# Kernel optimization log

Hardware: AMD Instinct MI355X
Metric: run time of the kernel (lower is better)

Reference implementation:

```python
import jax, jax.numpy as jnp
import numpy as np

NUM_HEADS = 16

def _rope_tables(T, head_dim):
    # angular_freq: (1/1024)**linspace(0,1,head_dim//4), padded with head_dim//4 zeros
    af = (1.0 / 1024.0) ** jnp.linspace(0.0, 1.0, head_dim // 4, dtype=jnp.float32)
    af = jnp.concatenate([af, jnp.zeros(head_dim // 4, dtype=jnp.float32)])  # [head_dim//2]
    t = jnp.arange(T, dtype=jnp.float32)
    theta = t[:, None] * af[None, :]  # [T, head_dim//2]
    return jnp.cos(theta), jnp.sin(theta)

def _apply_rope(x_bthd, cos, sin):
    # x_bthd: [B,T,H,D]; cos/sin: [T,D//2]
    x1, x2 = jnp.split(x_bthd.astype(jnp.float32), 2, axis=-1)
    c = cos[None, :, None, :]
    s = sin[None, :, None, :]
    y1 = x1 * c + x2 * s
    y2 = -x1 * s + x2 * c
    return jnp.concatenate([y1, y2], axis=-1).astype(x_bthd.dtype)

def setup_inputs() -> dict:
    key = jax.random.key(0)
    k1, k2, k3 = jax.random.split(key, 3)
    B, T, C = 4, 2048, 1024
    std = 0.5 * C ** (-0.5)
    bound = (3.0 ** 0.5) * std
    x = jax.random.normal(k1, (B, T, C), dtype=jnp.float32)
    qkv_w = jax.random.uniform(k2, (3, C, C), dtype=jnp.float32, minval=-bound, maxval=bound)
    c_proj_w = 0.02 * jax.random.normal(k3, (C, C), dtype=jnp.float32)
    c_proj_b = jnp.zeros((C,), dtype=jnp.float32)
    return {"x": x, "qkv_w": qkv_w, "c_proj_w": c_proj_w, "c_proj_b": c_proj_b}

def reference(x, qkv_w, c_proj_w, c_proj_b):
    B, T, C = x.shape
    H = NUM_HEADS
    D = C // H
    # QKV projection: F.linear(x, qkv_w.flatten(end_dim=1)) -> x @ W.T
    qkv = jnp.einsum('btc,nc->btn', x, qkv_w.reshape(3 * C, C))  # [B,T,3C]
    qkv = qkv.reshape(B, T, 3 * H, D)
    q, k, v = jnp.split(qkv, 3, axis=-2)  # each [B,T,H,D]
    cos, sin = _rope_tables(T, D)
    q = _apply_rope(q, cos, sin)
    k = _apply_rope(k, cos, sin)
    # causal SDPA, scale 1/sqrt(D)
    scale = 1.0 / jnp.sqrt(jnp.float32(D))
    scores = jnp.einsum('bqhd,bkhd->bhqk', q, k) * scale  # [B,H,T,T]
    mask = jnp.tril(jnp.ones((T, T), dtype=bool))
    scores = jnp.where(mask[None, None], scores, jnp.finfo(scores.dtype).min)
    attn = jax.nn.softmax(scores, axis=-1)
    y = jnp.einsum('bhqk,bkhd->bqhd', attn, v).reshape(B, T, C)
    return y @ c_proj_w.T + c_proj_b
```

## Files before the change

kernel.cpp:

```cpp
#include <hip/hip_runtime.h>

typedef unsigned short ushort_t;
typedef __bf16 bf16x8 __attribute__((ext_vector_type(8)));
typedef unsigned short ushort8_t __attribute__((ext_vector_type(8)));
typedef unsigned short ushort4_t __attribute__((ext_vector_type(4)));
typedef float floatx4 __attribute__((ext_vector_type(4)));
typedef unsigned int uint4_t __attribute__((ext_vector_type(4)));
typedef unsigned int uint2_t __attribute__((ext_vector_type(2)));

__device__ __forceinline__ ushort_t f2bf(float f) {
    unsigned int u = __float_as_uint(f);
    u += 0x7FFFu + ((u >> 16) & 1u);
    return (ushort_t)(u >> 16);
}
__device__ __forceinline__ float bf2f(ushort_t b) {
    return __uint_as_float(((unsigned int)b) << 16);
}
__device__ __forceinline__ bf16x8 ld_frag(const ushort_t* p) {
    ushort8_t u = *(const ushort8_t*)p;
    return __builtin_bit_cast(bf16x8, u);
}
__device__ __forceinline__ unsigned pack_trunc(float lo, float hi) {
    return __builtin_amdgcn_perm(__float_as_uint(hi), __float_as_uint(lo), 0x07060302u);
}
__device__ __forceinline__ floatx4 mfma16(bf16x8 a, bf16x8 b, floatx4 c) {
    return __builtin_amdgcn_mfma_f32_16x16x32_bf16(a, b, c, 0, 0, 0);
}
__device__ __forceinline__ void async16(const ushort_t* g, ushort_t* l) {
    __builtin_amdgcn_global_load_lds((const __attribute__((address_space(1))) void*)g,
                                     (__attribute__((address_space(3))) void*)l, 16, 0, 0);
}

__global__ __launch_bounds__(256) void cvt_bf16(const float* __restrict__ src,
                                                ushort_t* __restrict__ dst, int n8) {
    int idx = blockIdx.x * 256 + threadIdx.x;
    if (idx >= n8) return;
    const float4* s = (const float4*)src + (size_t)idx * 2;
    float4 a = s[0], b = s[1];
    ushort8_t v;
    v[0] = f2bf(a.x); v[1] = f2bf(a.y); v[2] = f2bf(a.z); v[3] = f2bf(a.w);
    v[4] = f2bf(b.x); v[5] = f2bf(b.y); v[6] = f2bf(b.z); v[7] = f2bf(b.w);
    *(ushort8_t*)(dst + (size_t)idx * 8) = v;
}

template <typename TB, int MODE>
__global__ __launch_bounds__(256) void gemm_a(const ushort_t* __restrict__ A,
                                              const TB* __restrict__ B,
                                              const float* __restrict__ bias,
                                              void* __restrict__ Cout,
                                              ushort_t* __restrict__ vt,
                                              int M, int N, int K) {
    constexpr bool BF16B = (sizeof(TB) == 2);
    __shared__ __attribute__((aligned(16))) ushort_t As[128 * 32];
    __shared__ __attribute__((aligned(16))) ushort_t Bs[128 * 32];
    const int tid = threadIdx.x;
    const int lane = tid & 63, wave = tid >> 6;
    const int quad = lane >> 4, l16 = lane & 15;
    const int wm = wave & 1, wn = wave >> 1;
    const int m0 = blockIdx.y * 128, n0 = blockIdx.x * 128;

    const ushort_t* ga = A + (size_t)(m0 + wave * 32 + (lane >> 2)) * K + (lane & 3) * 8;
    ushort_t* la = As + wave * 1024;
    const ushort_t* gb16 = nullptr;
    if constexpr (BF16B)
        gb16 = (const ushort_t*)B + (size_t)(n0 + wave * 32 + (lane >> 2)) * K + (lane & 3) * 8;
    ushort_t* lb = Bs + wave * 1024;

    floatx4 acc[4][4] = {};

    for (int k0 = 0; k0 < K; k0 += 32) {
        __syncthreads();
        async16(ga + k0, la);
        async16(ga + k0 + (size_t)16 * K, la + 512);
        if constexpr (BF16B) {
            async16(gb16 + k0, lb);
            async16(gb16 + k0 + (size_t)16 * K, lb + 512);
        } else {
#pragma unroll
            for (int it = 0; it < 4; ++it) {
                int linear = it * 256 + tid;
                int row = linear >> 3, c = (linear & 7) * 4;
                const float* src = (const float*)B + (size_t)(n0 + row) * K + k0 + c;
                float4 f = *(const float4*)src;
                ushort4_t v;
                v.x = f2bf(f.x); v.y = f2bf(f.y); v.z = f2bf(f.z); v.w = f2bf(f.w);
                *(ushort4_t*)&Bs[row * 32 + c] = v;
            }
        }
        __syncthreads();

        bf16x8 af[4], bfr[4];
#pragma unroll
        for (int mt = 0; mt < 4; ++mt)
            af[mt] = ld_frag(&As[(wm * 64 + mt * 16 + l16) * 32 + quad * 8]);
#pragma unroll
        for (int nt = 0; nt < 4; ++nt)
            bfr[nt] = ld_frag(&Bs[(wn * 64 + nt * 16 + l16) * 32 + quad * 8]);
#pragma unroll
        for (int mt = 0; mt < 4; ++mt)
#pragma unroll
            for (int nt = 0; nt < 4; ++nt)
                acc[mt][nt] = mfma16(af[mt], bfr[nt], acc[mt][nt]);
    }

    if constexpr (MODE == 2) {
        if (n0 + wn * 64 < 2048) {
            float afreq = exp2f((float)l16 * (-10.0f / 15.0f));
#pragma unroll
            for (int mt = 0; mt < 4; ++mt) {
                int rowb = m0 + wm * 64 + mt * 16 + quad * 4;
#pragma unroll
                for (int r = 0; r < 4; ++r) {
                    int t = (rowb + r) & 2047;
                    float th = (float)t * afreq;
                    float sn = sinf(th), cs = cosf(th);
                    float q1 = acc[mt][0][r], q2 = acc[mt][2][r];
                    acc[mt][0][r] = q1 * cs + q2 * sn;
                    acc[mt][2][r] = -q1 * sn + q2 * cs;
                }
            }
        }
    }

#pragma unroll
    for (int mt = 0; mt < 4; ++mt) {
        int row = m0 + wm * 64 + mt * 16 + quad * 4;
#pragma unroll
        for (int nt = 0; nt < 4; ++nt) {
            int nglob = n0 + wn * 64 + nt * 16 + l16;
            if constexpr (MODE == 0) {
                float bv = bias ? bias[nglob] : 0.0f;
#pragma unroll
                for (int r = 0; r < 4; ++r)
                    ((float*)Cout)[(size_t)(row + r) * N + nglob] = acc[mt][nt][r] + bv;
            } else {
                if (nglob < 2048) {
#pragma unroll
                    for (int r = 0; r < 4; ++r)
                        ((ushort_t*)Cout)[(size_t)(row + r) * 2048 + nglob] =
                            f2bf(acc[mt][nt][r]);
                } else {
                    int d = nglob & 63, hh = (nglob >> 6) & 15;
                    int bb = row >> 11, t = row & 2047;
                    ushort4_t pk;
                    pk.x = f2bf(acc[mt][nt][0]);
                    pk.y = f2bf(acc[mt][nt][1]);
                    pk.z = f2bf(acc[mt][nt][2]);
                    pk.w = f2bf(acc[mt][nt][3]);
                    *(ushort4_t*)&vt[(((size_t)bb * 16 + hh) * 64 + d) * 2048 + t] = pk;
                }
            }
        }
    }
}

#define ATT_SCALE 0.18033688011112042f

template <bool DIAG>
__device__ __forceinline__ void attn_step(
    const ushort_t* __restrict__ Ks, const ushort_t* __restrict__ Vt,
    ushort_t* __restrict__ Pw, const bf16x8 (&qf)[2][2],
    floatx4 (&o)[2][4], floatx4 (&lac)[2], float (&m_)[2],
    int quad, int l16, int sw8, int mhi, int qrel) {
    ushort8_t ou;
#pragma unroll
    for (int j = 0; j < 8; ++j) ou[j] = 0x3F80;
    const bf16x8 vONE = __builtin_bit_cast(bf16x8, ou);

    floatx4 s[8][2];
#pragma unroll
    for (int mt = 0; mt < 8; ++mt) {
        if (DIAG && mt > mhi) continue;
        const ushort_t* kr = &Ks[(mt * 16 + l16) * 64];
        bf16x8 k0 = ld_frag(kr + ((quad * 8) ^ sw8));
        bf16x8 k1 = ld_frag(kr + ((32 + quad * 8) ^ sw8));
#pragma unroll
        for (int nt = 0; nt < 2; ++nt) {
            floatx4 z = {};
            z = mfma16(k0, qf[nt][0], z);
            s[mt][nt] = mfma16(k1, qf[nt][1], z);
        }
    }
    if (DIAG) {
#pragma unroll
        for (int mt = 0; mt < 8; ++mt) {
            if (mt > mhi) continue;
#pragma unroll
            for (int nt = 0; nt < 2; ++nt)
#pragma unroll
                for (int r = 0; r < 4; ++r)
                    if (mt * 16 + quad * 4 + r > qrel + nt * 16 + l16)
                        s[mt][nt][r] = -3e38f;
        }
    }
    float alpha_l[2];
#pragma unroll
    for (int nt = 0; nt < 2; ++nt) {
        float mx = -3e38f;
#pragma unroll
        for (int mt = 0; mt < 8; ++mt) {
            if (DIAG && mt > mhi) continue;
            mx = fmaxf(mx, fmaxf(fmaxf(s[mt][nt][0], s[mt][nt][1]),
                                 fmaxf(s[mt][nt][2], s[mt][nt][3])));
        }
        mx = fmaxf(mx, __shfl_xor(mx, 16));
        mx = fmaxf(mx, __shfl_xor(mx, 32));
        float mnew = fmaxf(m_[nt], mx);
        alpha_l[nt] = __builtin_amdgcn_exp2f(m_[nt] - mnew);
        m_[nt] = mnew;
#pragma unroll
        for (int mt = 0; mt < 8; ++mt) {
            if (DIAG && mt > mhi) continue;
#pragma unroll
            for (int r = 0; r < 4; ++r)
                s[mt][nt][r] = __builtin_amdgcn_exp2f(s[mt][nt][r] - mnew);
        }
    }
#pragma unroll
    for (int mtq = 0; mtq < 2; ++mtq)
#pragma unroll
        for (int r = 0; r < 4; ++r) {
            float ao = __shfl(alpha_l[mtq], quad * 4 + r);
            lac[mtq][r] *= ao;
#pragma unroll
            for (int ntd = 0; ntd < 4; ++ntd) o[mtq][ntd][r] *= ao;
        }
#pragma unroll
    for (int mt = 0; mt < 8; ++mt) {
        if (DIAG && mt > mhi) continue;
#pragma unroll
        for (int nt = 0; nt < 2; ++nt) {
            uint2_t pk;
            pk.x = pack_trunc(s[mt][nt][0], s[mt][nt][1]);
            pk.y = pack_trunc(s[mt][nt][2], s[mt][nt][3]);
            *(uint2_t*)&Pw[(nt * 16 + l16) * 136 + mt * 16 + quad * 4] = pk;
        }
    }
#pragma unroll
    for (int kc = 0; kc < 4; ++kc) {
        if (DIAG && kc > (mhi >> 1)) continue;
        bf16x8 ap0 = ld_frag(&Pw[l16 * 136 + kc * 32 + quad * 8]);
        bf16x8 ap1 = ld_frag(&Pw[(16 + l16) * 136 + kc * 32 + quad * 8]);
        lac[0] = mfma16(ap0, vONE, lac[0]);
        lac[1] = mfma16(ap1, vONE, lac[1]);
#pragma unroll
        for (int ntd = 0; ntd < 4; ++ntd) {
            bf16x8 bv = ld_frag(&Vt[(ntd * 16 + l16) * 136 + kc * 32 + quad * 8]);
            o[0][ntd] = mfma16(ap0, bv, o[0][ntd]);
            o[1][ntd] = mfma16(ap1, bv, o[1][ntd]);
        }
    }
}

__global__ __launch_bounds__(256, 2) void attn_kernel(const ushort_t* __restrict__ qk,
                                                      const ushort_t* __restrict__ vt,
                                                      ushort_t* __restrict__ y) {
    __shared__ __attribute__((aligned(16))) ushort_t lds[34304];
    ushort_t* Ks = lds;
    ushort_t* Vt = lds + 8192;
    ushort_t* Pw0 = lds + 16896;

    const int tid = threadIdx.x, lane = tid & 63, w = tid >> 6;
    const int quad = lane >> 4, l16 = lane & 15;
    const int lrow = lane >> 3, lchunk = lane & 7;
    const int sw8 = 8 * (l16 >> 1);
    const int bh = (int)blockIdx.x >> 3, j = (int)blockIdx.x & 7;
    const int b = bh >> 4, h = bh & 15;
    ushort_t* Pw = Pw0 + w * 4352;

    const ushort_t* base_k = qk + (size_t)(b * 2048) * 2048 + 1024 + h * 64;
    const ushort_t* base_v = vt + (size_t)bh * 64 * 2048;

#pragma unroll 1
    for (int ph = 0; ph < 2; ++ph) {
        const int jj = ph ? (15 - j) : j;
        const int q0 = jj * 128 + w * 32;

        bf16x8 qf[2][2];
        {
            const ushort_t* qb = qk + (size_t)(b * 2048 + q0) * 2048 + h * 64 + quad * 8;
#pragma unroll
            for (int nt = 0; nt < 2; ++nt)
#pragma unroll
                for (int kd = 0; kd < 2; ++kd) {
                    ushort8_t raw =
                        *(const ushort8_t*)(qb + (size_t)(nt * 16 + l16) * 2048 + kd * 32);
                    uint4_t dw;
#pragma unroll
                    for (int jx = 0; jx < 4; ++jx) {
                        float f0 = bf2f(raw[2 * jx]) * ATT_SCALE;
                        float f1 = bf2f(raw[2 * jx + 1]) * ATT_SCALE;
                        dw[jx] = pack_trunc(f0, f1);
                    }
                    qf[nt][kd] = __builtin_bit_cast(bf16x8, dw);
                }
        }

        floatx4 o[2][4] = {};
        floatx4 lac[2] = {};
        float m_[2] = {-3e38f, -3e38f};

#pragma unroll 1
        for (int kt = 0; kt <= jj; ++kt) {
            __syncthreads();
            {
                const ushort_t* gk = base_k + (size_t)(kt * 128) * 2048 + lchunk * 8;
#pragma unroll
                for (int i = 0; i < 4; ++i) {
                    int row = w * 32 + i * 8 + lrow;
                    ushort8_t v = *(const ushort8_t*)(gk + (size_t)row * 2048);
                    *(ushort8_t*)&Ks[row * 64 + 8 * (lchunk ^ ((row >> 1) & 7))] = v;
                }
            }
            {
                const ushort_t* gv = base_v + kt * 128;
#pragma unroll
                for (int i = 0; i < 4; ++i) {
                    int linear = i * 256 + tid;
                    int d = linear >> 4, c8 = linear & 15;
                    ushort8_t v = *(const ushort8_t*)(gv + (size_t)d * 2048 + c8 * 8);
                    *(ushort8_t*)&Vt[d * 136 + c8 * 8] = v;
                }
            }
            __syncthreads();

            if (kt < jj)
                attn_step<false>(Ks, Vt, Pw, qf, o, lac, m_, quad, l16, sw8, 7, 0);
            else
                attn_step<true>(Ks, Vt, Pw, qf, o, lac, m_, quad, l16, sw8,
                                2 * w + 1, w * 32);
        }

        ushort_t* yb = y + (size_t)(b * 2048 + q0) * 1024 + h * 64;
#pragma unroll
        for (int mtq = 0; mtq < 2; ++mtq)
#pragma unroll
            for (int r = 0; r < 4; ++r) {
                float inv = 1.0f / lac[mtq][r];
                int row = mtq * 16 + quad * 4 + r;
#pragma unroll
                for (int ntd = 0; ntd < 4; ++ntd)
                    yb[(size_t)row * 1024 + ntd * 16 + l16] = f2bf(o[mtq][ntd][r] * inv);
            }
    }
}

extern "C" void kernel_launch(void* const* d_in, const int* in_sizes, int n_in,
                              void* d_out, int out_size, void* d_ws, size_t ws_size,
                              hipStream_t stream) {
    const float* x = (const float*)d_in[0];
    const float* qkv_w = (const float*)d_in[1];
    const float* c_proj_w = (const float*)d_in[2];
    const float* c_proj_b = (const float*)d_in[3];
    float* out = (float*)d_out;

    const int M = 8192;

    ushort_t* qk = (ushort_t*)d_ws;
    ushort_t* vt = (ushort_t*)((char*)d_ws + (size_t)33554432);
    ushort_t* wpb = vt;
    ushort_t* xb = (ushort_t*)((char*)d_ws + (size_t)50331648);
    ushort_t* y = xb;

    cvt_bf16<<<dim3(4096), 256, 0, stream>>>(x, xb, M * 1024 / 8);

    gemm_a<float, 2><<<dim3(3072 / 128, M / 128), 256, 0, stream>>>(
        xb, qkv_w, nullptr, qk, vt, M, 3072, 1024);

    attn_kernel<<<dim3(512), 256, 0, stream>>>(qk, vt, y);

    cvt_bf16<<<dim3(512), 256, 0, stream>>>(c_proj_w, wpb, 1024 * 1024 / 8);

    gemm_a<ushort_t, 0><<<dim3(1024 / 128, M / 128), 256, 0, stream>>>(
        y, wpb, c_proj_b, out, nullptr, M, 1024, 1024);
}
```

Baseline: 308.4 us.

## Pre-convert QKV weights to bf16, prefetch K/V tiles in registers, use fast sincos

The QKV weight matrix is now converted to bf16 in a separate pass, so the QKV GEMM loads both operands with async global-to-LDS copies instead of converting fp32 B tiles inline on every k-step. The bf16 copy of x is staged in the output buffer to free workspace for the weights. The attention kernel now loads the next K/V tile into registers while the current tile is being computed, so global latency overlaps with compute at the cost of extra registers. RoPE switches to the fast __sincosf intrinsic, which is less accurate for large angles.

```diff
diff --git a/kernel.cpp b/kernel.cpp
--- a/kernel.cpp
+++ b/kernel.cpp
@@ -43,14 +43,13 @@
     *(ushort8_t*)(dst + (size_t)idx * 8) = v;
 }
 
-template <typename TB, int MODE>
+template <int MODE>
 __global__ __launch_bounds__(256) void gemm_a(const ushort_t* __restrict__ A,
-                                              const TB* __restrict__ B,
+                                              const ushort_t* __restrict__ B,
                                               const float* __restrict__ bias,
                                               void* __restrict__ Cout,
                                               ushort_t* __restrict__ vt,
                                               int M, int N, int K) {
-    constexpr bool BF16B = (sizeof(TB) == 2);
     __shared__ __attribute__((aligned(16))) ushort_t As[128 * 32];
     __shared__ __attribute__((aligned(16))) ushort_t Bs[128 * 32];
     const int tid = threadIdx.x;
@@ -60,10 +59,8 @@
     const int m0 = blockIdx.y * 128, n0 = blockIdx.x * 128;
 
     const ushort_t* ga = A + (size_t)(m0 + wave * 32 + (lane >> 2)) * K + (lane & 3) * 8;
+    const ushort_t* gb = B + (size_t)(n0 + wave * 32 + (lane >> 2)) * K + (lane & 3) * 8;
     ushort_t* la = As + wave * 1024;
-    const ushort_t* gb16 = nullptr;
-    if constexpr (BF16B)
-        gb16 = (const ushort_t*)B + (size_t)(n0 + wave * 32 + (lane >> 2)) * K + (lane & 3) * 8;
     ushort_t* lb = Bs + wave * 1024;
 
     floatx4 acc[4][4] = {};
@@ -72,21 +69,8 @@
         __syncthreads();
         async16(ga + k0, la);
         async16(ga + k0 + (size_t)16 * K, la + 512);
-        if constexpr (BF16B) {
-            async16(gb16 + k0, lb);
-            async16(gb16 + k0 + (size_t)16 * K, lb + 512);
-        } else {
-#pragma unroll
-            for (int it = 0; it < 4; ++it) {
-                int linear = it * 256 + tid;
-                int row = linear >> 3, c = (linear & 7) * 4;
-                const float* src = (const float*)B + (size_t)(n0 + row) * K + k0 + c;
-                float4 f = *(const float4*)src;
-                ushort4_t v;
-                v.x = f2bf(f.x); v.y = f2bf(f.y); v.z = f2bf(f.z); v.w = f2bf(f.w);
-                *(ushort4_t*)&Bs[row * 32 + c] = v;
-            }
-        }
+        async16(gb + k0, lb);
+        async16(gb + k0 + (size_t)16 * K, lb + 512);
         __syncthreads();
 
         bf16x8 af[4], bfr[4];
@@ -113,7 +97,8 @@
                 for (int r = 0; r < 4; ++r) {
                     int t = (rowb + r) & 2047;
                     float th = (float)t * afreq;
-                    float sn = sinf(th), cs = cosf(th);
+                    float sn, cs;
+                    __sincosf(th, &sn, &cs);
                     float q1 = acc[mt][0][r], q2 = acc[mt][2][r];
                     acc[mt][0][r] = q1 * cs + q2 * sn;
                     acc[mt][2][r] = -q1 * sn + q2 * cs;
@@ -270,6 +255,30 @@
 
     const ushort_t* base_k = qk + (size_t)(b * 2048) * 2048 + 1024 + h * 64;
     const ushort_t* base_v = vt + (size_t)bh * 64 * 2048;
+    const int vd = w * 4 + (lane >> 4);
+    const int vc8 = lane & 15;
+
+    ushort8_t kreg[4], vreg[4];
+    auto load_kv = [&](int kt) {
+        const ushort_t* gk = base_k + (size_t)(kt * 128) * 2048 + lchunk * 8;
+#pragma unroll
+        for (int i = 0; i < 4; ++i)
+            kreg[i] = *(const ushort8_t*)(gk + (size_t)(w * 32 + i * 8 + lrow) * 2048);
+        const ushort_t* gv = base_v + kt * 128;
+#pragma unroll
+        for (int i = 0; i < 4; ++i)
+            vreg[i] = *(const ushort8_t*)(gv + (size_t)(i * 16 + vd) * 2048 + vc8 * 8);
+    };
+    auto store_kv = [&]() {
+#pragma unroll
+        for (int i = 0; i < 4; ++i) {
+            int row = w * 32 + i * 8 + lrow;
+            *(ushort8_t*)&Ks[row * 64 + 8 * (lchunk ^ ((row >> 1) & 7))] = kreg[i];
+        }
+#pragma unroll
+        for (int i = 0; i < 4; ++i)
+            *(ushort8_t*)&Vt[(i * 16 + vd) * 136 + vc8 * 8] = vreg[i];
+    };
 
 #pragma unroll 1
     for (int ph = 0; ph < 2; ++ph) {
@@ -300,29 +309,13 @@
         floatx4 lac[2] = {};
         float m_[2] = {-3e38f, -3e38f};
 
+        load_kv(0);
 #pragma unroll 1
         for (int kt = 0; kt <= jj; ++kt) {
             __syncthreads();
-            {
-                const ushort_t* gk = base_k + (size_t)(kt * 128) * 2048 + lchunk * 8;
-#pragma unroll
-                for (int i = 0; i < 4; ++i) {
-                    int row = w * 32 + i * 8 + lrow;
-                    ushort8_t v = *(const ushort8_t*)(gk + (size_t)row * 2048);
-                    *(ushort8_t*)&Ks[row * 64 + 8 * (lchunk ^ ((row >> 1) & 7))] = v;
-                }
-            }
-            {
-                const ushort_t* gv = base_v + kt * 128;
-#pragma unroll
-                for (int i = 0; i < 4; ++i) {
-                    int linear = i * 256 + tid;
-                    int d = linear >> 4, c8 = linear & 15;
-                    ushort8_t v = *(const ushort8_t*)(gv + (size_t)d * 2048 + c8 * 8);
-                    *(ushort8_t*)&Vt[d * 136 + c8 * 8] = v;
-                }
-            }
+            store_kv();
             __syncthreads();
+            if (kt < jj) load_kv(kt + 1);
 
             if (kt < jj)
                 attn_step<false>(Ks, Vt, Pw, qf, o, lac, m_, quad, l16, sw8, 7, 0);
@@ -359,18 +352,20 @@
     ushort_t* qk = (ushort_t*)d_ws;
     ushort_t* vt = (ushort_t*)((char*)d_ws + (size_t)33554432);
     ushort_t* wpb = vt;
-    ushort_t* xb = (ushort_t*)((char*)d_ws + (size_t)50331648);
-    ushort_t* y = xb;
+    ushort_t* wb = (ushort_t*)((char*)d_ws + (size_t)50331648);
+    ushort_t* y = wb;
+    ushort_t* xb = (ushort_t*)d_out;
 
     cvt_bf16<<<dim3(4096), 256, 0, stream>>>(x, xb, M * 1024 / 8);
-
-    gemm_a<float, 2><<<dim3(3072 / 128, M / 128), 256, 0, stream>>>(
-        xb, qkv_w, nullptr, qk, vt, M, 3072, 1024);
+    cvt_bf16<<<dim3(1536), 256, 0, stream>>>(qkv_w, wb, 3072 * 1024 / 8);
+
+    gemm_a<2><<<dim3(3072 / 128, M / 128), 256, 0, stream>>>(
+        xb, wb, nullptr, qk, vt, M, 3072, 1024);
 
     attn_kernel<<<dim3(512), 256, 0, stream>>>(qk, vt, y);
 
     cvt_bf16<<<dim3(512), 256, 0, stream>>>(c_proj_w, wpb, 1024 * 1024 / 8);
 
-    gemm_a<ushort_t, 0><<<dim3(1024 / 128, M / 128), 256, 0, stream>>>(
+    gemm_a<0><<<dim3(1024 / 128, M / 128), 256, 0, stream>>>(
         y, wpb, c_proj_b, out, nullptr, M, 1024, 1024);
 }
```

Result: faster. 273.2 us (-11.4%).
